# Kernel optimization log

Hardware: AMD Instinct MI355X
Metric: run time of the kernel (lower is better)

The kernel has to match this reference:

```python
import jax, jax.numpy as jnp
import numpy as np

IN_FEATURES = 4096
OUT_FEATURES = 4096
NUM_GROUPS = 32
HARDTANH_MIN = -2.0
HARDTANH_MAX = 2.0
EPS = 1e-6


def setup_inputs() -> dict:
    key = jax.random.key(0)
    k1, k2 = jax.random.split(key)
    x = jax.random.normal(k1, (8192, IN_FEATURES), dtype=jnp.float32)
    W = jax.random.normal(k2, (OUT_FEATURES, IN_FEATURES), dtype=jnp.float32)
    b = jnp.zeros((OUT_FEATURES,), dtype=jnp.float32)
    return {"x": x, "W": W, "b": b}


def reference(x, W, b):
    B = x.shape[0]
    group_size = OUT_FEATURES // NUM_GROUPS
    # GEMM: y[b, n] = sum_k x[b, k] * W[n, k]
    y = jnp.einsum("bk,nk->bn", x, W)
    # GroupNorm over each group of channels per row (no affine scale)
    yg = y.reshape(B, NUM_GROUPS, group_size)
    mean = jnp.mean(yg, axis=2, keepdims=True)
    var = jnp.mean((yg - mean) ** 2, axis=2, keepdims=True)
    norm = (yg - mean) / jnp.sqrt(var + EPS)
    norm = norm.reshape(B, OUT_FEATURES) + b[None, :]
    # kernel clamps to [-2, 2], then outer clamp to [hardtanh_min, hardtanh_max]
    out = jnp.clip(norm, -2.0, 2.0)
    out = jnp.clip(out, HARDTANH_MIN, HARDTANH_MAX)
    return out
```

## Files before the change

kernel.cpp:

```cpp
#include <hip/hip_runtime.h>
#include <hip/hip_bf16.h>
#include <stdint.h>

#define M_DIM 8192
#define N_DIM 4096
#define K_DIM 4096
#define BM 256
#define BN 256
#define BK 64
#define NTL 64

typedef __attribute__((ext_vector_type(8))) short short8;
typedef __attribute__((ext_vector_type(4))) float f32x4;
typedef unsigned short ushort_t;

#define SBAR()  asm volatile("s_barrier" ::: "memory")
#define LGKM(n) asm volatile("s_waitcnt lgkmcnt(" #n ")" ::: "memory")
#define VM(n)   asm volatile("s_waitcnt vmcnt(" #n ")" ::: "memory")
#define SCHEDB() __builtin_amdgcn_sched_barrier(0)

__device__ __forceinline__ ushort_t f2bf(float f) {
    uint32_t u = __float_as_uint(f);
    uint32_t r = (u + 0x7FFFu + ((u >> 16) & 1u)) >> 16;
    return (ushort_t)r;
}

__global__ void cvt_f32_bf16(const float4* __restrict__ in, ushort* __restrict__ out4, int n4) {
    int i = blockIdx.x * blockDim.x + threadIdx.x;
    if (i < n4) {
        float4 v = in[i];
        ushort_t a = f2bf(v.x), b = f2bf(v.y), c = f2bf(v.z), d = f2bf(v.w);
        uint32_t lo = (uint32_t)a | ((uint32_t)b << 16);
        uint32_t hi = (uint32_t)c | ((uint32_t)d << 16);
        uint2* o = reinterpret_cast<uint2*>(out4);
        o[i] = make_uint2(lo, hi);
    }
}

__device__ __forceinline__ void gload_lds16(const ushort_t* g, void* l) {
    __builtin_amdgcn_global_load_lds(
        (const __attribute__((address_space(1))) unsigned int*)g,
        (__attribute__((address_space(3))) unsigned int*)l,
        16, 0, 0);
}

__global__ __launch_bounds__(512, 2)
void gemm_gn_kernel(const ushort_t* __restrict__ xb,
                    const ushort_t* __restrict__ wb,
                    const float*   __restrict__ bias,
                    float*         __restrict__ out)
{
    __shared__ char pool[131072];

    const int tid = threadIdx.x;
    const int w   = tid >> 6;
    const int l   = tid & 63;
    const int wr  = w >> 2;
    const int wc  = w & 3;
    const int l15 = l & 15;
    const int l4  = l >> 4;

    const int TN = N_DIM / BN;
    int bid = blockIdx.x;
    bid = (bid & 7) * 64 + (bid >> 3);
    const int brow = (bid / TN) * BM;
    const int bcol = (bid % TN) * BN;

    const int srow8 = tid >> 3;
    const int sslot = (tid & 7) ^ (srow8 & 7);
    const ushort_t* gA = xb + (size_t)(brow + srow8) * K_DIM + sslot * 8;
    const ushort_t* gB = wb + (size_t)(bcol + srow8) * K_DIM + sslot * 8;
    const size_t ROW64 = (size_t)64 * K_DIM;
    const int w1024 = w * 1024;

    auto STAGE_A = [&](int buf, int half, int kt) {
        const ushort_t* s = gA + (size_t)half * 128 * K_DIM + (size_t)kt * 64;
        char* d = pool + buf * 65536 + half * 16384 + w1024;
        gload_lds16(s,         d);
        gload_lds16(s + ROW64, d + 8192);
    };
    auto STAGE_B = [&](int buf, int half, int kt) {
        const ushort_t* s = gB + (size_t)half * 128 * K_DIM + (size_t)kt * 64;
        char* d = pool + buf * 65536 + 32768 + half * 16384 + w1024;
        gload_lds16(s,         d);
        gload_lds16(s + ROW64, d + 8192);
    };

    const int swz = (l15 & 7) << 4;
    const int x0  = (l4 * 16) ^ swz;
    const int x1  = (64 + l4 * 16) ^ swz;

    short8 afL[8], afH[8], bfL[4], bfH[4];

    auto RD_A = [&](short8* dst, const char* Ab, int mi0) {
#pragma unroll
        for (int m = 0; m < 4; ++m) {
            const char* p = Ab + ((mi0 + m) * 32 + wr * 16 + l15) * 128;
            dst[m * 2]     = *(const short8*)(p + x0);
            dst[m * 2 + 1] = *(const short8*)(p + x1);
        }
    };
    auto RD_B = [&](short8* dst, const char* Bb, int ni0) {
#pragma unroll
        for (int n = 0; n < 2; ++n) {
            const char* p = Bb + ((ni0 + n) * 64 + wc * 16 + l15) * 128;
            dst[n * 2]     = *(const short8*)(p + x0);
            dst[n * 2 + 1] = *(const short8*)(p + x1);
        }
    };

    f32x4 acc[8][4];
#pragma unroll
    for (int i = 0; i < 8; ++i)
#pragma unroll
        for (int j = 0; j < 4; ++j) acc[i][j] = (f32x4){0.f, 0.f, 0.f, 0.f};

    auto MM = [&](short8* A, short8* B, int m0, int n0) {
#pragma unroll
        for (int k = 0; k < 2; ++k)
#pragma unroll
            for (int m = 0; m < 4; ++m)
#pragma unroll
                for (int n = 0; n < 2; ++n)
                    acc[m0 + m][n0 + n] = __builtin_amdgcn_mfma_f32_16x16x32_bf16(
                        A[m * 2 + k], B[n * 2 + k], acc[m0 + m][n0 + n], 0, 0, 0);
    };

    STAGE_A(0, 0, 0); STAGE_A(0, 1, 0);
    STAGE_B(0, 0, 0); STAGE_B(0, 1, 0);
    STAGE_A(1, 0, 1); STAGE_A(1, 1, 1);
    STAGE_B(1, 0, 1);
    VM(6);
    SBAR();

#pragma unroll 2
    for (int T = 0; T < NTL; ++T) {
        const int c = T & 1;
        const char* Ab = pool + c * 65536;
        const char* Bb = Ab + 32768;

        RD_A(afL, Ab, 0);
        RD_B(bfL, Bb, 0);
        if (T + 1 < NTL) STAGE_B(c ^ 1, 1, T + 1);
        LGKM(8);
        SBAR(); LGKM(0); SCHEDB();
        __builtin_amdgcn_s_setprio(1);
        MM(afL, bfL, 0, 0);
        __builtin_amdgcn_s_setprio(0);
        SBAR();

        RD_A(afH, Ab, 4);
        if (T + 2 < NTL) STAGE_A(c, 0, T + 2);
        SBAR(); LGKM(0); SCHEDB();
        __builtin_amdgcn_s_setprio(1);
        MM(afH, bfL, 4, 0);
        __builtin_amdgcn_s_setprio(0);
        SBAR();

        RD_B(bfH, Bb, 2);
        if (T + 2 < NTL) STAGE_A(c, 1, T + 2);
        SBAR(); LGKM(0); SCHEDB();
        __builtin_amdgcn_s_setprio(1);
        MM(afH, bfH, 4, 2);
        __builtin_amdgcn_s_setprio(0);
        SBAR();

        if (T + 2 < NTL) STAGE_B(c, 0, T + 2);
        if (T < NTL - 2) { VM(6); } else { VM(0); }
        SBAR(); SCHEDB();
        __builtin_amdgcn_s_setprio(1);
        MM(afL, bfH, 0, 2);
        __builtin_amdgcn_s_setprio(0);
        SBAR();
    }

    float* redS  = (float*)pool;
    float* redS2 = (float*)(pool + 8192);
#pragma unroll
    for (int mi = 0; mi < 8; ++mi)
#pragma unroll
        for (int r = 0; r < 4; ++r) {
            float gl  = acc[mi][0][r] + acc[mi][1][r];
            float gh  = acc[mi][2][r] + acc[mi][3][r];
            float gl2 = acc[mi][0][r] * acc[mi][0][r] + acc[mi][1][r] * acc[mi][1][r];
            float gh2 = acc[mi][2][r] * acc[mi][2][r] + acc[mi][3][r] * acc[mi][3][r];
#pragma unroll
            for (int m = 1; m < 16; m <<= 1) {
                gl  += __shfl_xor(gl,  m);
                gh  += __shfl_xor(gh,  m);
                gl2 += __shfl_xor(gl2, m);
                gh2 += __shfl_xor(gh2, m);
            }
            if (l15 == 0) {
                int R = mi * 32 + wr * 16 + l4 * 4 + r;
                redS [R * 8 + wc * 2]     = gl;
                redS [R * 8 + wc * 2 + 1] = gh;
                redS2[R * 8 + wc * 2]     = gl2;
                redS2[R * 8 + wc * 2 + 1] = gh2;
            }
        }
    __syncthreads();

    float bv[4];
#pragma unroll
    for (int ni = 0; ni < 4; ++ni)
        bv[ni] = bias[bcol + ni * 64 + wc * 16 + l15];

    const float inv_gs = 1.0f / 128.0f;
#pragma unroll
    for (int mi = 0; mi < 8; ++mi)
#pragma unroll
        for (int r = 0; r < 4; ++r) {
            int R = mi * 32 + wr * 16 + l4 * 4 + r;
            float S0 = redS [R * 8 + 0] + redS [R * 8 + 2] + redS [R * 8 + 4] + redS [R * 8 + 6];
            float S1 = redS [R * 8 + 1] + redS [R * 8 + 3] + redS [R * 8 + 5] + redS [R * 8 + 7];
            float T0 = redS2[R * 8 + 0] + redS2[R * 8 + 2] + redS2[R * 8 + 4] + redS2[R * 8 + 6];
            float T1 = redS2[R * 8 + 1] + redS2[R * 8 + 3] + redS2[R * 8 + 5] + redS2[R * 8 + 7];
            float mean0 = S0 * inv_gs, mean1 = S1 * inv_gs;
            float inv0 = rsqrtf(T0 * inv_gs - mean0 * mean0 + 1e-6f);
            float inv1 = rsqrtf(T1 * inv_gs - mean1 * mean1 + 1e-6f);
            size_t rowbase = (size_t)(brow + R) * N_DIM + bcol + wc * 16 + l15;
#pragma unroll
            for (int ni = 0; ni < 4; ++ni) {
                float mean = (ni < 2) ? mean0 : mean1;
                float inv  = (ni < 2) ? inv0  : inv1;
                float v = (acc[mi][ni][r] - mean) * inv + bv[ni];
                v = fminf(fmaxf(v, -2.0f), 2.0f);
                out[rowbase + ni * 64] = v;
            }
        }
}

extern "C" void kernel_launch(void* const* d_in, const int* in_sizes, int n_in,
                              void* d_out, int out_size, void* d_ws, size_t ws_size,
                              hipStream_t stream) {
    const float* x = (const float*)d_in[0];
    const float* W = (const float*)d_in[1];
    const float* b = (const float*)d_in[2];
    float* out = (float*)d_out;

    ushort_t* xb = (ushort_t*)d_ws;
    ushort_t* wb = xb + (size_t)M_DIM * K_DIM;

    int n4x = M_DIM * K_DIM / 4;
    cvt_f32_bf16<<<(n4x + 255) / 256, 256, 0, stream>>>(
        (const float4*)x, xb, n4x);
    int n4w = N_DIM * K_DIM / 4;
    cvt_f32_bf16<<<(n4w + 255) / 256, 256, 0, stream>>>(
        (const float4*)W, wb, n4w);

    int grid = (M_DIM / BM) * (N_DIM / BN);
    gemm_gn_kernel<<<grid, 512, 0, stream>>>(xb, wb, b, out);
}
```

Baseline: 324.2 us.

## Restructure GEMM main loop to one barrier per tile with fragment prefetch

The K-loop is reorganized so each tile iteration uses a single workgroup barrier instead of five. LDS fragment reads for the next tile are issued while the MFMAs of the current tile are still running, and the global-to-LDS staging for tile T+2 is issued in larger batches after that one barrier. The MFMA quadrants are reordered to fit this schedule, and the priority raise moves inside the MM helper. The aim is to cut barrier stalls and hide LDS read latency behind matrix math, at the cost of a full vmcnt(0) wait each iteration and more live fragment registers.

```diff
diff --git a/kernel.cpp b/kernel.cpp
--- a/kernel.cpp
+++ b/kernel.cpp
@@ -116,6 +116,7 @@
         for (int j = 0; j < 4; ++j) acc[i][j] = (f32x4){0.f, 0.f, 0.f, 0.f};
 
     auto MM = [&](short8* A, short8* B, int m0, int n0) {
+        __builtin_amdgcn_s_setprio(1);
 #pragma unroll
         for (int k = 0; k < 2; ++k)
 #pragma unroll
@@ -124,55 +125,52 @@
                 for (int n = 0; n < 2; ++n)
                     acc[m0 + m][n0 + n] = __builtin_amdgcn_mfma_f32_16x16x32_bf16(
                         A[m * 2 + k], B[n * 2 + k], acc[m0 + m][n0 + n], 0, 0, 0);
-    };
-
-    STAGE_A(0, 0, 0); STAGE_A(0, 1, 0);
-    STAGE_B(0, 0, 0); STAGE_B(0, 1, 0);
-    STAGE_A(1, 0, 1); STAGE_A(1, 1, 1);
-    STAGE_B(1, 0, 1);
-    VM(6);
+        __builtin_amdgcn_s_setprio(0);
+    };
+
+    STAGE_A(0, 0, 0); STAGE_A(0, 1, 0); STAGE_B(0, 0, 0); STAGE_B(0, 1, 0);
+    STAGE_A(1, 0, 1); STAGE_A(1, 1, 1); STAGE_B(1, 0, 1); STAGE_B(1, 1, 1);
+    VM(8);
     SBAR();
+    RD_A(afL, pool, 0);
+    RD_B(bfL, pool + 32768, 0);
+    SCHEDB();
 
 #pragma unroll 2
     for (int T = 0; T < NTL; ++T) {
         const int c = T & 1;
-        const char* Ab = pool + c * 65536;
-        const char* Bb = Ab + 32768;
-
-        RD_A(afL, Ab, 0);
-        RD_B(bfL, Bb, 0);
-        if (T + 1 < NTL) STAGE_B(c ^ 1, 1, T + 1);
+        const char* Cur = pool + c * 65536;
+        const char* Nxt = pool + (c ^ 1) * 65536;
+
+        RD_B(bfH, Cur + 32768, 2);
+        SCHEDB();
+        LGKM(4);
+        SCHEDB();
+        MM(afL, bfL, 0, 0);
+
+        RD_A(afH, Cur, 4);
+        SCHEDB();
         LGKM(8);
-        SBAR(); LGKM(0); SCHEDB();
-        __builtin_amdgcn_s_setprio(1);
-        MM(afL, bfL, 0, 0);
-        __builtin_amdgcn_s_setprio(0);
+        SCHEDB();
+        MM(afL, bfH, 0, 2);
+
+        LGKM(0);
+        VM(0);
+        SCHEDB();
         SBAR();
-
-        RD_A(afH, Ab, 4);
-        if (T + 2 < NTL) STAGE_A(c, 0, T + 2);
-        SBAR(); LGKM(0); SCHEDB();
-        __builtin_amdgcn_s_setprio(1);
+        if (T + 2 < NTL) { STAGE_A(c, 0, T + 2); STAGE_A(c, 1, T + 2); }
+        if (T + 1 < NTL) RD_A(afL, Nxt, 0);
+        SCHEDB();
+        MM(afH, bfH, 4, 2);
+
+        if (T + 2 < NTL) { STAGE_B(c, 0, T + 2); STAGE_B(c, 1, T + 2); }
+        SCHEDB();
         MM(afH, bfL, 4, 0);
-        __builtin_amdgcn_s_setprio(0);
-        SBAR();
-
-        RD_B(bfH, Bb, 2);
-        if (T + 2 < NTL) STAGE_A(c, 1, T + 2);
-        SBAR(); LGKM(0); SCHEDB();
-        __builtin_amdgcn_s_setprio(1);
-        MM(afH, bfH, 4, 2);
-        __builtin_amdgcn_s_setprio(0);
-        SBAR();
-
-        if (T + 2 < NTL) STAGE_B(c, 0, T + 2);
-        if (T < NTL - 2) { VM(6); } else { VM(0); }
-        SBAR(); SCHEDB();
-        __builtin_amdgcn_s_setprio(1);
-        MM(afL, bfH, 0, 2);
-        __builtin_amdgcn_s_setprio(0);
-        SBAR();
+        if (T + 1 < NTL) RD_B(bfL, Nxt + 32768, 0);
+        SCHEDB();
     }
+
+    __syncthreads();
 
     float* redS  = (float*)pool;
     float* redS2 = (float*)(pool + 8192);
```

After: 753.3 us. 132% more time.
